# Optimization experiments

Measured on AMD Instinct MI355X. Metric: run time of the kernel, lower is better.

Reference implementation:

```python
import jax, jax.numpy as jnp
import numpy as np
import math

B, S, D, H = 2, 2048, 1024, 16
DK = D // H  # 64
THETA = 500000.0


def setup_inputs() -> dict:
    key = jax.random.key(0)
    ks = jax.random.split(key, 6)
    x = jax.random.normal(ks[0], (B, S, D), dtype=jnp.float32)
    # RoPE frequencies: inv_freq = theta^{-(2i/dk)}, angles = pos * inv_freq
    inv_freq = 1.0 / (THETA ** (jnp.arange(0, DK, 2, dtype=jnp.float32) / DK))  # [DK/2]
    angles = jnp.arange(S, dtype=jnp.float32)[:, None] * inv_freq[None, :]      # [S, DK/2]
    freqs_cos = jnp.cos(angles)
    freqs_sin = jnp.sin(angles)
    # causal additive mask [B, S, S]: 0 on/below diagonal, -1e9 above
    causal = jnp.tril(jnp.ones((S, S), dtype=bool))
    mask = jnp.where(causal, 0.0, -1e9).astype(jnp.float32)
    mask = jnp.broadcast_to(mask, (B, S, S))
    scale = 0.02
    wq = jax.random.normal(ks[1], (D, D), dtype=jnp.float32) * scale
    wk = jax.random.normal(ks[2], (D, D), dtype=jnp.float32) * scale
    wv = jax.random.normal(ks[3], (D, D), dtype=jnp.float32) * scale
    wo = jax.random.normal(ks[4], (D, D), dtype=jnp.float32) * scale
    return {"x": x, "freqs_cos": freqs_cos, "freqs_sin": freqs_sin,
            "mask": mask, "wq": wq, "wk": wk, "wv": wv, "wo": wo}


def _apply_rope(t, cos, sin):
    # t: [B, S, H, DK]; cos/sin: [S, DK/2]
    tr = t.reshape(*t.shape[:-1], DK // 2, 2)
    t0, t1 = tr[..., 0], tr[..., 1]
    c = cos[None, :, None, :]
    s = sin[None, :, None, :]
    out = jnp.stack([t0 * c - t1 * s, t0 * s + t1 * c], axis=-1)
    return out.reshape(*t.shape)


def reference(x, freqs_cos, freqs_sin, mask, wq, wk, wv, wo):
    b, s, d = x.shape
    # nn.Linear(bias=False): y = x @ W^T, W is [out, in]
    q = jnp.einsum('bsd,ed->bse', x, wq).reshape(b, s, H, DK)
    k = jnp.einsum('bsd,ed->bse', x, wk).reshape(b, s, H, DK)
    v = jnp.einsum('bsd,ed->bse', x, wv).reshape(b, s, H, DK)
    q = _apply_rope(q, freqs_cos, freqs_sin)
    k = _apply_rope(k, freqs_cos, freqs_sin)
    inv_sqrt_dk = 1.0 / math.sqrt(DK)
    # scores: [B, H, S, S]
    scores = jnp.einsum('bqhd,bkhd->bhqk', q, k) * inv_sqrt_dk
    scores = scores + mask[:, None, :, :]
    # NOTE: the original module divides by sqrt(d_k) a SECOND time before softmax
    attn = jax.nn.softmax(scores * inv_sqrt_dk, axis=-1)
    out = jnp.einsum('bhqk,bkhd->bqhd', attn, v).reshape(b, s, d)
    return jnp.einsum('bsd,ed->bse', out, wo)
```

## Files before the change

### kernel.cpp

```cpp
#include <hip/hip_runtime.h>
#include <stdint.h>

#define Bq 2
#define Sq 2048
#define Dq 1024
#define Hq 16
#define DKq 64

typedef unsigned short u16;
typedef __attribute__((ext_vector_type(8))) __bf16 bf8;
typedef __attribute__((ext_vector_type(4))) __bf16 bf4;
typedef __attribute__((ext_vector_type(4))) float fx4;
typedef __attribute__((ext_vector_type(8))) unsigned short us8;
typedef __attribute__((ext_vector_type(4))) unsigned short us4;

__device__ __forceinline__ u16 f2bf(float f) {
    union { float f; unsigned int i; } v; v.f = f;
    unsigned int r = v.i + 0x7FFFu + ((v.i >> 16) & 1u);
    return (u16)(r >> 16);
}

__device__ __forceinline__ void gll16(const void* g, void* l) {
    typedef __attribute__((address_space(1))) void GV;
    typedef __attribute__((address_space(3))) void LV;
    __builtin_amdgcn_global_load_lds((GV*)g, (LV*)l, 16, 0, 0);
}

template<int N> __device__ __forceinline__ void waitv() {
    asm volatile("s_waitcnt vmcnt(%0)" :: "n"(N) : "memory");
}

__global__ void __launch_bounds__(256) cvt_all(const float* __restrict__ x,
                                               const float* __restrict__ wq,
                                               const float* __restrict__ wk,
                                               const float* __restrict__ wv,
                                               const float* __restrict__ wo,
                                               u16* __restrict__ ws) {
    int blk = blockIdx.x;
    const float* s;
    u16* d;
    int i;
    if (blk < 4096)      { s = x;  d = ws;           i = blk * 256 + threadIdx.x; }
    else if (blk < 5120) { s = wq; d = ws + 4194304; i = (blk - 4096) * 256 + threadIdx.x; }
    else if (blk < 6144) { s = wk; d = ws + 5242880; i = (blk - 5120) * 256 + threadIdx.x; }
    else if (blk < 7168) { s = wv; d = ws + 6291456; i = (blk - 6144) * 256 + threadIdx.x; }
    else                 { s = wo; d = ws + 7340032; i = (blk - 7168) * 256 + threadIdx.x; }
    float4 v = *(const float4*)(s + (size_t)i * 4);
    us4 o;
    o[0] = f2bf(v.x); o[1] = f2bf(v.y); o[2] = f2bf(v.z); o[3] = f2bf(v.w);
    *(us4*)(d + (size_t)i * 4) = o;
}

template<int MODE>
__global__ void __launch_bounds__(256) gemm_bt(
    const u16* __restrict__ A,
    const u16* __restrict__ W0, const u16* __restrict__ W1, const u16* __restrict__ W2,
    u16* __restrict__ O0, u16* __restrict__ O1, u16* __restrict__ O2,
    float* __restrict__ Of,
    const float* __restrict__ fc, const float* __restrict__ fs)
{
    constexpr int K = 1024;
    constexpr int NT = K / 32;
    __shared__ __align__(16) u16 As[3][128 * 32];
    __shared__ __align__(16) u16 Bs[3][128 * 32];
    const int tid = threadIdx.x;
    const int lane = tid & 63, wid = tid >> 6;
    const int wr = wid >> 1, wc = wid & 1;
    const int fr = lane & 15, fq = lane >> 4;

    int L = blockIdx.x + 8 * (blockIdx.y + 32 * blockIdx.z);
    int chunk = gridDim.z * 4;
    int X = L & 7, C = L >> 3;
    int bx = C & 7;
    int P = X * chunk + (C >> 3);
    int by = P & 31, bz = P >> 5;
    const int m0 = by * 128, n0 = bx * 128;

    const u16* Wm = W0;
    u16* Ob = O0;
    if (MODE == 1) {
        if (bz == 1)      { Wm = W1; Ob = O1; }
        else if (bz == 2) { Wm = W2; Ob = O2; }
    }

    const int arow = tid >> 2;
    const int acol = (tid & 3) * 8;
    const u16* ga = A  + (size_t)(m0 + arow) * K + acol;
    const u16* gb = Wm + (size_t)(n0 + arow) * K + acol;

    fx4 acc[4][4] = {};

    auto STAGE = [&](int t, int bufi) {
        const u16* gan = ga + t * 32;
        const u16* gbn = gb + t * 32;
        gll16(gan,          As[bufi] + tid * 8);
        gll16(gan + 64 * K, As[bufi] + tid * 8 + 2048);
        gll16(gbn,          Bs[bufi] + tid * 8);
        gll16(gbn + 64 * K, Bs[bufi] + tid * 8 + 2048);
    };
    auto COMPUTE = [&](int bufi) {
        bf8 af[4], bfv[4];
        #pragma unroll
        for (int i = 0; i < 4; ++i)
            af[i] = *(const bf8*)(&As[bufi][(wr * 64 + i * 16 + fr) * 32 + fq * 8]);
        #pragma unroll
        for (int j = 0; j < 4; ++j)
            bfv[j] = *(const bf8*)(&Bs[bufi][(wc * 64 + j * 16 + fr) * 32 + fq * 8]);
        #pragma unroll
        for (int i = 0; i < 4; ++i)
            #pragma unroll
            for (int j = 0; j < 4; ++j)
                acc[i][j] = __builtin_amdgcn_mfma_f32_16x16x32_bf16(af[i], bfv[j], acc[i][j], 0, 0, 0);
    };

    STAGE(0, 0); STAGE(1, 1); STAGE(2, 2);

    int cur = 0;
    #pragma unroll 1
    for (int t = 0; t < NT - 2; ++t) {
        waitv<8>();
        __builtin_amdgcn_sched_barrier(0);
        __builtin_amdgcn_s_barrier();
        __builtin_amdgcn_sched_barrier(0);
        COMPUTE(cur);
        __builtin_amdgcn_sched_barrier(0);
        __builtin_amdgcn_s_barrier();
        __builtin_amdgcn_sched_barrier(0);
        if (t < NT - 3) STAGE(t + 3, cur);
        cur = cur == 2 ? 0 : cur + 1;
    }
    waitv<4>();
    __builtin_amdgcn_sched_barrier(0);
    __builtin_amdgcn_s_barrier();
    __builtin_amdgcn_sched_barrier(0);
    COMPUTE(cur);
    cur = cur == 2 ? 0 : cur + 1;
    waitv<0>();
    __builtin_amdgcn_sched_barrier(0);
    __builtin_amdgcn_s_barrier();
    __builtin_amdgcn_sched_barrier(0);
    COMPUTE(cur);

    if (MODE == 0) {
        #pragma unroll
        for (int i = 0; i < 4; ++i)
            #pragma unroll
            for (int j = 0; j < 4; ++j)
                #pragma unroll
                for (int r = 0; r < 4; ++r) {
                    int m = m0 + wr * 64 + i * 16 + fq * 4 + r;
                    int n = n0 + wc * 64 + j * 16 + fr;
                    Of[(size_t)m * 1024 + n] = acc[i][j][r];
                }
    } else if (bz == 2) {
        #pragma unroll
        for (int i = 0; i < 4; ++i)
            #pragma unroll
            for (int j = 0; j < 4; ++j) {
                int n = n0 + wc * 64 + j * 16 + fr;
                int mb = m0 + wr * 64 + i * 16 + fq * 4;
                int b = mb >> 11, s = mb & 2047;
                int h = n >> 6, dk = n & 63;
                bf4 pk;
                #pragma unroll
                for (int r = 0; r < 4; ++r) pk[r] = (__bf16)acc[i][j][r];
                *(bf4*)((__bf16*)Ob + (((size_t)(b * Hq + h)) * DKq + dk) * Sq + s) = pk;
            }
    } else {
        #pragma unroll
        for (int i = 0; i < 4; ++i)
            #pragma unroll
            for (int j = 0; j < 4; ++j) {
                int n = n0 + wc * 64 + j * 16 + fr;
                int h = n >> 6, dk = n & 63;
                int ip = dk >> 1;
                float sgn = (dk & 1) ? 1.f : -1.f;
                #pragma unroll
                for (int r = 0; r < 4; ++r) {
                    int m = m0 + wr * 64 + i * 16 + fq * 4 + r;
                    int b = m >> 11, s = m & 2047;
                    float v = acc[i][j][r];
                    float pv = __shfl_xor(v, 1);
                    float c  = fc[s * 32 + ip];
                    float sn = fs[s * 32 + ip];
                    float o = v * c + sgn * pv * sn;
                    ((__bf16*)Ob)[(((size_t)(b * Hq + h)) * Sq + s) * DKq + dk] = (__bf16)o;
                }
            }
    }
}

__device__ __forceinline__ int swz(int row) { return ((row & 7) ^ ((row >> 3) & 7)) << 4; }

__global__ void __launch_bounds__(512, 4) attn_k(const u16* __restrict__ Q,
                                                 const u16* __restrict__ Kg,
                                                 const u16* __restrict__ Vtg,
                                                 u16* __restrict__ AO) {
    int L = blockIdx.x + 32 * blockIdx.y;
    int X = L & 7, C = L >> 3;
    const int bh = X * 4 + (C & 3);
    const int Qt = 31 - (C >> 2);
    const int b = bh >> 4, h = bh & 15;
    const int tid = threadIdx.x, lane = tid & 63, wid = tid >> 6;
    const int wq4 = wid & 3, par = wid >> 2;
    const int fr = lane & 15, fq = lane >> 4;
    const int swzfr = swz(fr);

    __shared__ __align__(16) u16 Ks[2][64 * 64];
    __shared__ __align__(16) u16 Vs[2][64 * 64];
    __shared__ __align__(16) u16 Ps[8][16 * 64];
    __shared__ float Lx[4][64];

    const u16* Kp = Kg  + (size_t)bh * Sq * 64;
    const u16* Vp = Vtg + (size_t)bh * 64 * Sq;
    const int q0 = Qt * 64;
    const int nt = Qt + 1;
    const int NS = (nt + 1) >> 1;

    bf8 qf0, qf1;
    {
        const u16* Qp = Q + ((size_t)bh * Sq + q0) * 64;
        int qr = wq4 * 16 + fr;
        qf0 = *(const bf8*)(Qp + qr * 64 + fq * 8);
        qf1 = *(const bf8*)(Qp + qr * 64 + fq * 8 + 32);
    }

    fx4 oacc[4] = {};
    float l_loc = 0.f;

    const int srow = tid >> 3;
    const int sce  = (tid & 7) * 8;
    const int ldst = srow * 128 + (((tid & 7) * 16) ^ swz(srow));

    us8 kreg[2], vreg[2];
    #pragma unroll
    for (int c = 0; c < 2; ++c) {
        int t = c < nt ? c : nt - 1;
        kreg[c] = *(const us8*)(Kp + ((size_t)t * 64 + srow) * 64 + sce);
        vreg[c] = *(const us8*)(Vp + (size_t)srow * Sq + t * 64 + sce);
    }
    #pragma unroll
    for (int c = 0; c < 2; ++c) {
        *(us8*)((char*)Ks[c] + ldst) = kreg[c];
        *(us8*)((char*)Vs[c] + ldst) = vreg[c];
    }
    if (NS > 1) {
        #pragma unroll
        for (int c = 0; c < 2; ++c) {
            int t = 2 + c < nt ? 2 + c : nt - 1;
            kreg[c] = *(const us8*)(Kp + ((size_t)t * 64 + srow) * 64 + sce);
            vreg[c] = *(const us8*)(Vp + (size_t)srow * Sq + t * 64 + sce);
        }
    }
    __syncthreads();

    #pragma unroll 1
    for (int sp = 0; sp < NS; ++sp) {
        const int t = 2 * sp + par;
        if (t < nt) {
            const char* Kb = (const char*)Ks[par];
            const char* Vb = (const char*)Vs[par];
            char* Pw = (char*)Ps[wid] + fr * 128;

            fx4 sf[4];
            __builtin_amdgcn_s_setprio(1);
            #pragma unroll
            for (int sj = 0; sj < 4; ++sj) {
                int krow = sj * 16 + fr;
                bf8 kf0 = *(const bf8*)(Kb + krow * 128 + ((fq * 16) ^ swz(krow)));
                bf8 kf1 = *(const bf8*)(Kb + krow * 128 + ((64 + fq * 16) ^ swz(krow)));
                fx4 a = {0.f, 0.f, 0.f, 0.f};
                a = __builtin_amdgcn_mfma_f32_16x16x32_bf16(kf0, qf0, a, 0, 0, 0);
                a = __builtin_amdgcn_mfma_f32_16x16x32_bf16(kf1, qf1, a, 0, 0, 0);
                sf[sj] = a;
            }
            __builtin_amdgcn_s_setprio(0);

            float pv[4][4];
            #pragma unroll
            for (int sj = 0; sj < 4; ++sj)
                #pragma unroll
                for (int r = 0; r < 4; ++r)
                    pv[sj][r] = __expf(sf[sj][r] * 0.015625f);
            if (t == Qt) {
                int ql = wq4 * 16 + fr;
                #pragma unroll
                for (int sj = 0; sj < 4; ++sj)
                    #pragma unroll
                    for (int r = 0; r < 4; ++r)
                        if (sj * 16 + fq * 4 + r > ql) pv[sj][r] = 0.f;
            }
            #pragma unroll
            for (int sj = 0; sj < 4; ++sj) {
                bf4 w;
                #pragma unroll
                for (int r = 0; r < 4; ++r) { w[r] = (__bf16)pv[sj][r]; l_loc += pv[sj][r]; }
                *(bf4*)(Pw + ((sj * 32 + fq * 8) ^ swzfr)) = w;
            }

            __builtin_amdgcn_s_setprio(1);
            #pragma unroll
            for (int kk = 0; kk < 2; ++kk) {
                bf8 pf = *(const bf8*)(Pw + ((kk * 64 + fq * 16) ^ swzfr));
                #pragma unroll
                for (int mf = 0; mf < 4; ++mf) {
                    int vrow = mf * 16 + fr;
                    bf8 vf = *(const bf8*)(Vb + vrow * 128 + ((kk * 64 + fq * 16) ^ swz(vrow)));
                    oacc[mf] = __builtin_amdgcn_mfma_f32_16x16x32_bf16(vf, pf, oacc[mf], 0, 0, 0);
                }
            }
            __builtin_amdgcn_s_setprio(0);
        }
        __syncthreads();
        if (sp + 1 < NS) {
            #pragma unroll
            for (int c = 0; c < 2; ++c) {
                *(us8*)((char*)Ks[c] + ldst) = kreg[c];
                *(us8*)((char*)Vs[c] + ldst) = vreg[c];
            }
            if (sp + 2 < NS) {
                #pragma unroll
                for (int c = 0; c < 2; ++c) {
                    int tt = 2 * (sp + 2) + c; if (tt > nt - 1) tt = nt - 1;
                    kreg[c] = *(const us8*)(Kp + ((size_t)tt * 64 + srow) * 64 + sce);
                    vreg[c] = *(const us8*)(Vp + (size_t)srow * Sq + tt * 64 + sce);
                }
            }
            __syncthreads();
        }
    }

    l_loc += __shfl_xor(l_loc, 16);
    l_loc += __shfl_xor(l_loc, 32);
    if (par == 1) {
        float* ob = (float*)Ps + wq4 * 1024;
        #pragma unroll
        for (int mf = 0; mf < 4; ++mf)
            *(fx4*)(ob + lane * 16 + mf * 4) = oacc[mf];
        Lx[wq4][lane] = l_loc;
    }
    __syncthreads();
    if (par == 0) {
        const float* ob = (float*)Ps + wq4 * 1024;
        float lt = l_loc + Lx[wq4][lane];
        float linv = __builtin_amdgcn_rcpf(lt);
        int s = q0 + wq4 * 16 + fr;
        #pragma unroll
        for (int mf = 0; mf < 4; ++mf) {
            fx4 oh = *(const fx4*)(ob + lane * 16 + mf * 4);
            bf4 pk;
            #pragma unroll
            for (int r = 0; r < 4; ++r) pk[r] = (__bf16)((oacc[mf][r] + oh[r]) * linv);
            *(bf4*)((__bf16*)AO + ((size_t)(b * Sq + s)) * Dq + h * 64 + mf * 16 + fq * 4) = pk;
        }
    }
}

extern "C" void kernel_launch(void* const* d_in, const int* in_sizes, int n_in,
                              void* d_out, int out_size, void* d_ws, size_t ws_size,
                              hipStream_t stream) {
    const float* x  = (const float*)d_in[0];
    const float* fc = (const float*)d_in[1];
    const float* fs = (const float*)d_in[2];
    const float* wq = (const float*)d_in[4];
    const float* wk = (const float*)d_in[5];
    const float* wv = (const float*)d_in[6];
    const float* wo = (const float*)d_in[7];
    float* out = (float*)d_out;

    u16* ws  = (u16*)d_ws;
    u16* xb  = ws;
    u16* wqb = ws + 4194304;
    u16* wkb = ws + 5242880;
    u16* wvb = ws + 6291456;
    u16* wob = ws + 7340032;
    u16* Qb  = ws + 8388608;
    u16* Kb  = ws + 12582912;
    u16* Vb  = ws + 16777216;
    u16* AOb = ws + 20971520;

    cvt_all<<<8192, 256, 0, stream>>>(x, wq, wk, wv, wo, ws);

    dim3 g1(8, 32, 3);
    gemm_bt<1><<<g1, 256, 0, stream>>>(xb, wqb, wkb, wvb, Qb, Kb, Vb, nullptr, fc, fs);

    dim3 g2(32, 32, 1);
    attn_k<<<g2, 512, 0, stream>>>(Qb, Kb, Vb, AOb);

    dim3 g3(8, 32, 1);
    gemm_bt<0><<<g3, 256, 0, stream>>>(AOb, wob, nullptr, nullptr, nullptr, nullptr, nullptr, out, nullptr, nullptr);
}
```

Before: 121.8 us.

## Enlarge GEMM tiles to 256x256 with 512-thread blocks and split-phase prefetch

```diff
diff --git a/kernel.cpp b/kernel.cpp
--- a/kernel.cpp
+++ b/kernel.cpp
@@ -52,7 +52,7 @@
 }
 
 template<int MODE>
-__global__ void __launch_bounds__(256) gemm_bt(
+__global__ void __launch_bounds__(512, 1) gemm_bt(
     const u16* __restrict__ A,
     const u16* __restrict__ W0, const u16* __restrict__ W1, const u16* __restrict__ W2,
     u16* __restrict__ O0, u16* __restrict__ O1, u16* __restrict__ O2,
@@ -60,21 +60,27 @@
     const float* __restrict__ fc, const float* __restrict__ fs)
 {
     constexpr int K = 1024;
-    constexpr int NT = K / 32;
-    __shared__ __align__(16) u16 As[3][128 * 32];
-    __shared__ __align__(16) u16 Bs[3][128 * 32];
+    constexpr int NT = 32;
+    __shared__ __align__(16) u16 As[3][256 * 32];
+    __shared__ __align__(16) u16 Bs[3][256 * 32];
     const int tid = threadIdx.x;
     const int lane = tid & 63, wid = tid >> 6;
-    const int wr = wid >> 1, wc = wid & 1;
+    const int wr = wid >> 2, wc = wid & 3;
     const int fr = lane & 15, fq = lane >> 4;
 
-    int L = blockIdx.x + 8 * (blockIdx.y + 32 * blockIdx.z);
-    int chunk = gridDim.z * 4;
-    int X = L & 7, C = L >> 3;
-    int bx = C & 7;
-    int P = X * chunk + (C >> 3);
-    int by = P & 31, bz = P >> 5;
-    const int m0 = by * 128, n0 = bx * 128;
+    int wgid = blockIdx.x;
+    int Xc = wgid & 7, jj = wgid >> 3;
+    int by, bx, bz;
+    if (MODE == 1) {
+        int T = Xc * 24 + jj;
+        by = T / 12;
+        int p = T - by * 12;
+        bz = p >> 2; bx = p & 3;
+    } else {
+        int T = Xc * 8 + jj;
+        by = T >> 2; bx = T & 3; bz = 0;
+    }
+    const int m0 = by * 256, n0 = bx * 256;
 
     const u16* Wm = W0;
     u16* Ob = O0;
@@ -83,103 +89,110 @@
         else if (bz == 2) { Wm = W2; Ob = O2; }
     }
 
-    const int arow = tid >> 2;
-    const int acol = (tid & 3) * 8;
-    const u16* ga = A  + (size_t)(m0 + arow) * K + acol;
-    const u16* gb = Wm + (size_t)(n0 + arow) * K + acol;
-
-    fx4 acc[4][4] = {};
-
-    auto STAGE = [&](int t, int bufi) {
-        const u16* gan = ga + t * 32;
-        const u16* gbn = gb + t * 32;
-        gll16(gan,          As[bufi] + tid * 8);
-        gll16(gan + 64 * K, As[bufi] + tid * 8 + 2048);
-        gll16(gbn,          Bs[bufi] + tid * 8);
-        gll16(gbn + 64 * K, Bs[bufi] + tid * 8 + 2048);
+    const u16* ga = A  + (size_t)(m0 + (tid >> 2)) * K + (tid & 3) * 8;
+    const u16* gb = Wm + (size_t)(n0 + (tid >> 2)) * K + (tid & 3) * 8;
+
+    fx4 acc[8][4] = {};
+
+    auto STAGE_A = [&](int t, int b) {
+        gll16(ga + t * 32,           As[b] + tid * 8);
+        gll16(ga + 128 * K + t * 32, As[b] + tid * 8 + 4096);
     };
-    auto COMPUTE = [&](int bufi) {
-        bf8 af[4], bfv[4];
-        #pragma unroll
-        for (int i = 0; i < 4; ++i)
-            af[i] = *(const bf8*)(&As[bufi][(wr * 64 + i * 16 + fr) * 32 + fq * 8]);
-        #pragma unroll
-        for (int j = 0; j < 4; ++j)
-            bfv[j] = *(const bf8*)(&Bs[bufi][(wc * 64 + j * 16 + fr) * 32 + fq * 8]);
-        #pragma unroll
-        for (int i = 0; i < 4; ++i)
-            #pragma unroll
-            for (int j = 0; j < 4; ++j)
-                acc[i][j] = __builtin_amdgcn_mfma_f32_16x16x32_bf16(af[i], bfv[j], acc[i][j], 0, 0, 0);
+    auto STAGE_B = [&](int t, int b) {
+        gll16(gb + t * 32,           Bs[b] + tid * 8);
+        gll16(gb + 128 * K + t * 32, Bs[b] + tid * 8 + 4096);
     };
 
-    STAGE(0, 0); STAGE(1, 1); STAGE(2, 2);
-
-    int cur = 0;
-    #pragma unroll 1
-    for (int t = 0; t < NT - 2; ++t) {
-        waitv<8>();
-        __builtin_amdgcn_sched_barrier(0);
-        __builtin_amdgcn_s_barrier();
-        __builtin_amdgcn_sched_barrier(0);
-        COMPUTE(cur);
-        __builtin_amdgcn_sched_barrier(0);
-        __builtin_amdgcn_s_barrier();
-        __builtin_amdgcn_sched_barrier(0);
-        if (t < NT - 3) STAGE(t + 3, cur);
-        cur = cur == 2 ? 0 : cur + 1;
-    }
+    STAGE_A(0, 0); STAGE_B(0, 0);
+    STAGE_A(1, 1); STAGE_B(1, 1);
     waitv<4>();
     __builtin_amdgcn_sched_barrier(0);
     __builtin_amdgcn_s_barrier();
     __builtin_amdgcn_sched_barrier(0);
-    COMPUTE(cur);
-    cur = cur == 2 ? 0 : cur + 1;
-    waitv<0>();
-    __builtin_amdgcn_sched_barrier(0);
-    __builtin_amdgcn_s_barrier();
-    __builtin_amdgcn_sched_barrier(0);
-    COMPUTE(cur);
+
+    int b0 = 0;
+    #pragma unroll 1
+    for (int t = 0; t < NT; ++t) {
+        const u16* Ab = As[b0];
+        const u16* Bb = Bs[b0];
+        const int bn = b0 + 2 >= 3 ? b0 - 1 : b0 + 2;
+        bf8 bfr[4];
+        #pragma unroll
+        for (int nj = 0; nj < 4; ++nj)
+            bfr[nj] = *(const bf8*)(&Bb[(wc * 64 + nj * 16 + fr) * 32 + fq * 8]);
+
+        #pragma unroll
+        for (int ph = 0; ph < 2; ++ph) {
+            bf8 af[4];
+            #pragma unroll
+            for (int mi = 0; mi < 4; ++mi)
+                af[mi] = *(const bf8*)(&Ab[(wr * 128 + ph * 64 + mi * 16 + fr) * 32 + fq * 8]);
+            if (t + 2 < NT) {
+                if (ph == 0) STAGE_A(t + 2, bn);
+                else         STAGE_B(t + 2, bn);
+            }
+            __builtin_amdgcn_sched_barrier(0);
+            __builtin_amdgcn_s_barrier();
+            __builtin_amdgcn_sched_barrier(0);
+            __builtin_amdgcn_s_setprio(1);
+            #pragma unroll
+            for (int mi = 0; mi < 4; ++mi)
+                #pragma unroll
+                for (int nj = 0; nj < 4; ++nj)
+                    acc[ph * 4 + mi][nj] = __builtin_amdgcn_mfma_f32_16x16x32_bf16(
+                        af[mi], bfr[nj], acc[ph * 4 + mi][nj], 0, 0, 0);
+            __builtin_amdgcn_s_setprio(0);
+            __builtin_amdgcn_sched_barrier(0);
+            if (ph == 1) {
+                if (t < NT - 2) waitv<4>();
+                else            waitv<0>();
+                __builtin_amdgcn_sched_barrier(0);
+            }
+            __builtin_amdgcn_s_barrier();
+            __builtin_amdgcn_sched_barrier(0);
+        }
+        b0 = b0 + 1 >= 3 ? 0 : b0 + 1;
+    }
 
     if (MODE == 0) {
         #pragma unroll
-        for (int i = 0; i < 4; ++i)
-            #pragma unroll
-            for (int j = 0; j < 4; ++j)
+        for (int mi = 0; mi < 8; ++mi)
+            #pragma unroll
+            for (int nj = 0; nj < 4; ++nj)
                 #pragma unroll
                 for (int r = 0; r < 4; ++r) {
-                    int m = m0 + wr * 64 + i * 16 + fq * 4 + r;
-                    int n = n0 + wc * 64 + j * 16 + fr;
-                    Of[(size_t)m * 1024 + n] = acc[i][j][r];
+                    int m = m0 + wr * 128 + mi * 16 + fq * 4 + r;
+                    int n = n0 + wc * 64 + nj * 16 + fr;
+                    Of[(size_t)m * 1024 + n] = acc[mi][nj][r];
                 }
     } else if (bz == 2) {
         #pragma unroll
-        for (int i = 0; i < 4; ++i)
-            #pragma unroll
-            for (int j = 0; j < 4; ++j) {
-                int n = n0 + wc * 64 + j * 16 + fr;
-                int mb = m0 + wr * 64 + i * 16 + fq * 4;
+        for (int mi = 0; mi < 8; ++mi)
+            #pragma unroll
+            for (int nj = 0; nj < 4; ++nj) {
+                int n = n0 + wc * 64 + nj * 16 + fr;
+                int mb = m0 + wr * 128 + mi * 16 + fq * 4;
                 int b = mb >> 11, s = mb & 2047;
                 int h = n >> 6, dk = n & 63;
                 bf4 pk;
                 #pragma unroll
-                for (int r = 0; r < 4; ++r) pk[r] = (__bf16)acc[i][j][r];
+                for (int r = 0; r < 4; ++r) pk[r] = (__bf16)acc[mi][nj][r];
                 *(bf4*)((__bf16*)Ob + (((size_t)(b * Hq + h)) * DKq + dk) * Sq + s) = pk;
             }
     } else {
         #pragma unroll
-        for (int i = 0; i < 4; ++i)
-            #pragma unroll
-            for (int j = 0; j < 4; ++j) {
-                int n = n0 + wc * 64 + j * 16 + fr;
+        for (int mi = 0; mi < 8; ++mi)
+            #pragma unroll
+            for (int nj = 0; nj < 4; ++nj) {
+                int n = n0 + wc * 64 + nj * 16 + fr;
                 int h = n >> 6, dk = n & 63;
                 int ip = dk >> 1;
                 float sgn = (dk & 1) ? 1.f : -1.f;
                 #pragma unroll
                 for (int r = 0; r < 4; ++r) {
-                    int m = m0 + wr * 64 + i * 16 + fq * 4 + r;
+                    int m = m0 + wr * 128 + mi * 16 + fq * 4 + r;
                     int b = m >> 11, s = m & 2047;
-                    float v = acc[i][j][r];
+                    float v = acc[mi][nj][r];
                     float pv = __shfl_xor(v, 1);
                     float c  = fc[s * 32 + ip];
                     float sn = fs[s * 32 + ip];
@@ -381,12 +394,10 @@
 
     cvt_all<<<8192, 256, 0, stream>>>(x, wq, wk, wv, wo, ws);
 
-    dim3 g1(8, 32, 3);
-    gemm_bt<1><<<g1, 256, 0, stream>>>(xb, wqb, wkb, wvb, Qb, Kb, Vb, nullptr, fc, fs);
+    gemm_bt<1><<<192, 512, 0, stream>>>(xb, wqb, wkb, wvb, Qb, Kb, Vb, nullptr, fc, fs);
 
     dim3 g2(32, 32, 1);
     attn_k<<<g2, 512, 0, stream>>>(Qb, Kb, Vb, AOb);
 
-    dim3 g3(8, 32, 1);
-    gemm_bt<0><<<g3, 256, 0, stream>>>(AOb, wob, nullptr, nullptr, nullptr, nullptr, nullptr, out, nullptr, nullptr);
-}
+    gemm_bt<0><<<64, 512, 0, stream>>>(AOb, wob, nullptr, nullptr, nullptr, nullptr, nullptr, out, nullptr, nullptr);
+}
```

New measurement: 128.1 us. 5.2% more time.
